# Kernel optimization log

Hardware: AMD Instinct MI355X
Metric: run time of the kernel (lower is better)

## Reference

```python
import jax, jax.numpy as jnp
import numpy as np

IMAGE_SIZE = 256
NEAR = 0.1
FAR = 100.0
CHUNK = 200  # faces per rasterization chunk


def setup_inputs() -> dict:
    key = jax.random.key(0)
    k1, k2, k3 = jax.random.split(key, 3)
    B, Nv, Nf = 1, 10000, 10000
    # vertices sized so that after weak projection (u = f*x + c, f=1015, c=112,
    # orig_size=224) they land inside the image plane; z kept positive.
    xy = jax.random.uniform(k1, (B, Nv, 2), minval=-0.1, maxval=0.1)
    z = jax.random.uniform(k3, (B, Nv, 1), minval=0.4, maxval=0.8)
    vertices = jnp.concatenate([xy, z], axis=-1).astype(jnp.float32)
    faces = jax.random.randint(k2, (B, Nf, 3), 0, Nv).astype(jnp.int64)
    f, c = 1015.0, 112.0
    K = jnp.broadcast_to(jnp.array([[f, 0.0, c], [0.0, f, c], [0.0, 0.0, 1.0]],
                                   dtype=jnp.float32), (B, 3, 3))
    R = jnp.broadcast_to(jnp.eye(3, dtype=jnp.float32), (B, 3, 3))
    t = jnp.zeros((B, 3), dtype=jnp.float32)
    return {"vertices": vertices, "faces": faces, "K": K, "R": R, "t": t,
            "orig_size": 224}


def weak_projection(vertices, K, R, t, orig_size):
    # camera transform: v_cam = v @ R^T + t   [B,N,3]
    v = jnp.einsum('bnj,bkj->bnk', vertices, R) + t[:, None, :]
    x, y, z = v[..., 0], v[..., 1], v[..., 2]
    fx, fy = K[:, 0:1, 0], K[:, 1:2, 1]  # [B,1]
    cx, cy = K[:, 0:1, 2], K[:, 1:2, 2]
    # weak (orthographic-with-focal) projection: no divide by z
    u = fx * x + cx
    w = fy * y + cy
    xn = 2.0 * u / orig_size - 1.0        # NDC x in [-1,1]
    yn = -(2.0 * w / orig_size - 1.0)     # image y down -> NDC y up
    return jnp.stack([xn, yn, z], axis=-1)


def _rasterize_depth(face_verts):
    # face_verts: [B, F, 3, 3] (NDC x, NDC y, camera z)
    B, F = face_verts.shape[0], face_verts.shape[1]
    IS = IMAGE_SIZE
    ps = (2.0 * (jnp.arange(IS, dtype=jnp.float32) + 0.5) / IS) - 1.0
    px = ps[None, :]    # [1, W]
    py = -ps[:, None]   # [H, 1], row 0 is top of image

    def chunk_depth(fc):  # fc: [B, C, 3, 3] -> per-pixel min depth [B, H, W]
        x = fc[..., 0][..., None, None]  # [B,C,3,1,1]
        y = fc[..., 1][..., None, None]
        z = fc[..., 2]                   # [B,C,3]
        dx0, dx1, dx2 = x[:, :, 0] - px, x[:, :, 1] - px, x[:, :, 2] - px  # [B,C,1,W]
        dy0, dy1, dy2 = y[:, :, 0] - py, y[:, :, 1] - py, y[:, :, 2] - py  # [B,C,H,1]
        # edge functions (unnormalized barycentric weights) [B,C,H,W]
        w0 = dx1 * dy2 - dx2 * dy1
        w1 = dx2 * dy0 - dx0 * dy2
        w2 = dx0 * dy1 - dx1 * dy0
        area = w0 + w1 + w2
        s = jnp.sign(area)
        inside = (w0 * s >= 0) & (w1 * s >= 0) & (w2 * s >= 0) & (jnp.abs(area) > 1e-10)
        safe_area = jnp.where(jnp.abs(area) > 1e-10, area, 1.0)
        zp = (w0 * z[:, :, 0, None, None] + w1 * z[:, :, 1, None, None]
              + w2 * z[:, :, 2, None, None]) / safe_area
        valid = inside & (zp > NEAR) & (zp < FAR)
        return jnp.min(jnp.where(valid, zp, FAR), axis=1)  # [B,H,W]

    pad = (-F) % CHUNK
    fv = jnp.pad(face_verts, ((0, 0), (0, pad), (0, 0), (0, 0)))  # degenerate pads -> area 0
    n = (F + pad) // CHUNK
    fv = fv.reshape(B, n, CHUNK, 3, 3).transpose(1, 0, 2, 3, 4)  # [n,B,C,3,3]
    ck = jax.checkpoint(chunk_depth)

    def step(carry, fc):
        return jnp.minimum(carry, ck(fc)), None

    depth0 = jnp.full((B, IS, IS), FAR, dtype=jnp.float32)
    depth, _ = jax.lax.scan(step, depth0, fv)
    return depth


def reference(vertices, faces, K, R, t, orig_size):
    # fill_back: append reversed-winding copies of every face
    faces2 = jnp.concatenate([faces, faces[:, :, ::-1]], axis=1)  # [B,2F,3]
    v = weak_projection(vertices, K, R, t, orig_size)             # [B,Nv,3]
    face_verts = jax.vmap(lambda vb, fb: vb[fb])(v, faces2)       # [B,2F,3,3]
    return _rasterize_depth(face_verts)                           # [B,256,256]
```

## Files before the change

kernel.cpp:

```cpp
#include <hip/hip_runtime.h>

#define IMG 256
#define FARZ 100.0f
#define FARB 0x42C80000u
#define TILE 16
#define NZ 8
#define RND 512
#define BT 512
#define EPS 1e-4f
#define EPSZ 1e-5f
#define DPIX (2.0f / IMG)
#define BBZ_EMPTY 0x00FF00FFu

typedef float f2 __attribute__((ext_vector_type(2)));
static __device__ __forceinline__ f2 pkfma(f2 a, f2 b, f2 c) {
    return __builtin_elementwise_fma(a, b, c);
}
static __device__ __forceinline__ f2 pkmin(f2 a, f2 b) {
    return __builtin_elementwise_min(a, b);
}
static __device__ __forceinline__ float wave_max(float v) {
#pragma unroll
    for (int m = 32; m >= 1; m >>= 1) v = fmaxf(v, __shfl_xor(v, m, 64));
    return v;
}
static __device__ __forceinline__ float wave_min(float v) {
#pragma unroll
    for (int m = 32; m >= 1; m >>= 1) v = fminf(v, __shfl_xor(v, m, 64));
    return v;
}

struct Q4 { f2 r0, r1; };
static __device__ __forceinline__ Q4 eval4(float A, float B, float C,
                                           float px0, float py0) {
    Q4 o;
    float w00 = fmaf(B, px0, fmaf(C, py0, A));
    o.r0 = pkfma((f2){B, B}, (f2){0.0f, DPIX}, (f2){w00, w00});
    o.r1 = pkfma((f2){C, C}, (f2){-DPIX, -DPIX}, o.r0);
    return o;
}

__global__ __launch_bounds__(256) void setup(const float* __restrict__ verts,
                                             const int* __restrict__ faces,
                                             const float* __restrict__ K,
                                             const float* __restrict__ Rm,
                                             const float* __restrict__ t,
                                             const int* __restrict__ osz,
                                             float4* __restrict__ QQ,
                                             float2* __restrict__ BBz,
                                             unsigned* __restrict__ gb,
                                             unsigned* __restrict__ out, int Nf) {
    __shared__ float sb[4][4];
    int tid = threadIdx.x;
    int i = blockIdx.x * 256 + tid;
    out[i] = FARB;

    float k0 = 104.0f, k1 = 104.0f, k2 = 104.0f, k3 = 104.0f;
    if (i < Nf) {
        float fx = K[0], cx = K[2], fy = K[4], cy = K[5];
        float os = (float)osz[0];
        float r00 = Rm[0], r01 = Rm[1], r02 = Rm[2];
        float r10 = Rm[3], r11 = Rm[4], r12 = Rm[5];
        float r20 = Rm[6], r21 = Rm[7], r22 = Rm[8];
        float t0 = t[0], t1 = t[1], t2 = t[2];

        float3 p[3];
#pragma unroll
        for (int k = 0; k < 3; ++k) {
            int vi = faces[3 * i + k];
            float vx = verts[3 * vi], vy = verts[3 * vi + 1], vz = verts[3 * vi + 2];
            float x = r00 * vx + r01 * vy + r02 * vz + t0;
            float y = r10 * vx + r11 * vy + r12 * vz + t1;
            float z = r20 * vx + r21 * vy + r22 * vz + t2;
            float u = fx * x + cx;
            float w = fy * y + cy;
            p[k].x = 2.0f * u / os - 1.0f;
            p[k].y = -(2.0f * w / os - 1.0f);
            p[k].z = z;
        }

        float A0 = p[1].x * p[2].y - p[2].x * p[1].y;
        float B0 = p[1].y - p[2].y;
        float C0 = p[2].x - p[1].x;
        float A1 = p[2].x * p[0].y - p[0].x * p[2].y;
        float B1 = p[2].y - p[0].y;
        float C1 = p[0].x - p[2].x;
        float A2 = p[0].x * p[1].y - p[1].x * p[0].y;
        float B2 = p[0].y - p[1].y;
        float C2 = p[1].x - p[0].x;

        float area = A0 + A1 + A2;
        if (fabsf(area) > 1e-10f) {
            float s = (area > 0.0f) ? 1.0f : -1.0f;
            A0 *= s; B0 *= s; C0 *= s;
            A1 *= s; B1 *= s; C1 *= s;
            A2 *= s; B2 *= s; C2 *= s;
            float inv = (1.0f / area) * s;
            float P = (A0 * p[0].z + A1 * p[1].z + A2 * p[2].z) * inv;
            float Q = (B0 * p[0].z + B1 * p[1].z + B2 * p[2].z) * inv;
            float Rr = (C0 * p[0].z + C1 * p[1].z + C2 * p[2].z) * inv;
            QQ[3 * i + 0] = make_float4(A0, B0, C0, A1);
            QQ[3 * i + 1] = make_float4(B1, C1, A2, B2);
            QQ[3 * i + 2] = make_float4(C2, P, Q, Rr);
            float xmn = fminf(p[0].x, fminf(p[1].x, p[2].x));
            float xmx = fmaxf(p[0].x, fmaxf(p[1].x, p[2].x));
            float ymn = fminf(p[0].y, fminf(p[1].y, p[2].y));
            float ymx = fmaxf(p[0].y, fmaxf(p[1].y, p[2].y));
            float zmv = fminf(p[0].z, fminf(p[1].z, p[2].z));
            int c0 = (int)floorf((xmn + 1.0f) * 128.0f - 0.52f);
            int c1 = (int)ceilf ((xmx + 1.0f) * 128.0f - 0.48f);
            int r0 = (int)floorf((1.0f - ymx) * 128.0f - 0.52f);
            int r1 = (int)ceilf ((1.0f - ymn) * 128.0f - 0.48f);
            c0 = min(max(c0, 0), 255); c1 = min(max(c1, 0), 255);
            r0 = min(max(r0, 0), 255); r1 = min(max(r1, 0), 255);
            unsigned bb = (unsigned)c0 | ((unsigned)c1 << 8) |
                          ((unsigned)r0 << 16) | ((unsigned)r1 << 24);
            BBz[i] = make_float2(__uint_as_float(bb), zmv);
            k0 = 4.0f + xmn; k1 = 4.0f - xmx;
            k2 = 4.0f + ymn; k3 = 4.0f - ymx;
        } else {
            QQ[3 * i + 0] = make_float4(0.0f, 0.0f, 0.0f, 0.0f);
            QQ[3 * i + 1] = make_float4(0.0f, 0.0f, 0.0f, 0.0f);
            QQ[3 * i + 2] = make_float4(0.0f, 0.0f, 0.0f, 0.0f);
            BBz[i] = make_float2(__uint_as_float(BBZ_EMPTY), 1e9f);
        }
    }

    k0 = wave_min(k0); k1 = wave_min(k1); k2 = wave_min(k2); k3 = wave_min(k3);
    int wave = tid >> 6, lane = tid & 63;
    if (lane == 0) { sb[wave][0] = k0; sb[wave][1] = k1; sb[wave][2] = k2; sb[wave][3] = k3; }
    __syncthreads();
    if (tid < 4) {
        float v = fminf(fminf(sb[0][tid], sb[1][tid]), fminf(sb[2][tid], sb[3][tid]));
        atomicMin(&gb[tid], __float_as_uint(v));
    }
}

__global__ __launch_bounds__(BT) void raster(const float4* __restrict__ QQ,
                                             const float2* __restrict__ BBz,
                                             const unsigned* __restrict__ gb,
                                             unsigned* __restrict__ out,
                                             int Nf, int span) {
    __shared__ float4 sf[RND * 3];
    __shared__ unsigned sdepth[TILE * TILE];
    __shared__ int scnt2[2];

    const int tid = threadIdx.x;
    const int bx = blockIdx.x, by = blockIdx.y;
    const int wave = tid >> 6, lane = tid & 63;
    const int tx0 = bx * TILE, ty0 = by * TILE;

    const float cx0 = -1.0f + (tx0 + 0.5f) * DPIX;
    const float cyTop = 1.0f - (ty0 + 0.5f) * DPIX;
    const float tcx = cx0 + 7.5f * DPIX;
    const float tcy = cyTop - 7.5f * DPIX;
    const float hx = 7.5f * DPIX;
    const float hy = 7.5f * DPIX;

    const float gxmin = __uint_as_float(gb[0]) - 4.0f;
    const float gxmax = 4.0f - __uint_as_float(gb[1]);
    const float gymin = __uint_as_float(gb[2]) - 4.0f;
    const float gymax = 4.0f - __uint_as_float(gb[3]);

    const int col = tid & 15, row = (tid >> 4) & 15;
    const int gidx = (ty0 + row) * IMG + tx0 + col;
    unsigned orig = FARB;
    if (tid < 256) {
        orig = out[gidx];
        sdepth[tid] = orig;
    }
    if (tid == 0) { scnt2[0] = 0; scnt2[1] = 0; }

    const int qx = (lane & 7) * 2, qy = (lane >> 3) * 2;
    const float fpx0 = cx0 + (float)qx * DPIX;
    const float fpy0 = cyTop - (float)qy * DPIX;
    int cm = 0;
    {
        const float x0 = fpx0, x1 = fpx0 + DPIX;
        const float y0 = fpy0, y1 = fpy0 - DPIX;
        const bool cx_0 = (x0 >= gxmin - 1e-6f) & (x0 <= gxmax + 1e-6f);
        const bool cx_1 = (x1 >= gxmin - 1e-6f) & (x1 <= gxmax + 1e-6f);
        const bool cy_0 = (y0 >= gymin - 1e-6f) & (y0 <= gymax + 1e-6f);
        const bool cy_1 = (y1 >= gymin - 1e-6f) & (y1 <= gymax + 1e-6f);
        cm = (cx_0 & cy_0) | ((cx_1 & cy_0) << 1) |
             ((cx_0 & cy_1) << 2) | ((cx_1 & cy_1) << 3);
    }
    __syncthreads();

    unsigned dmu[4];
    float T;
    {
        uint2 a = *(const uint2*)&sdepth[qy * TILE + qx];
        uint2 b = *(const uint2*)&sdepth[(qy + 1) * TILE + qx];
        dmu[0] = a.x; dmu[1] = a.y; dmu[2] = b.x; dmu[3] = b.y;
        float m = 0.0f;
        if (cm & 1) m = fmaxf(m, __uint_as_float(a.x));
        if (cm & 2) m = fmaxf(m, __uint_as_float(a.y));
        if (cm & 4) m = fmaxf(m, __uint_as_float(b.x));
        if (cm & 8) m = fmaxf(m, __uint_as_float(b.y));
        T = wave_max(m);
    }
    if (T == 0.0f) return;

    const int fbase = blockIdx.z * span;
    const int fend = min(fbase + span, Nf);

    int f = fbase + tid;
    float2 bz = (f < fend) ? BBz[f]
                           : make_float2(__uint_as_float(BBZ_EMPTY), 1e9f);

    int p = 0;
    for (int base = fbase; base < fend; base += RND) {
        const unsigned bb = __float_as_uint(bz.x);
        const bool pre = ((int)(bb & 255u) <= tx0 + 15) &
                         ((int)((bb >> 8) & 255u) >= tx0) &
                         ((int)((bb >> 16) & 255u) <= ty0 + 15) &
                         ((int)(bb >> 24) >= ty0) &
                         (bz.y <= T + EPSZ);
        const int fcur = f;
        const int fn = f + RND;
        bz = (fn < fend) ? BBz[fn]
                         : make_float2(__uint_as_float(BBZ_EMPTY), 1e9f);

        bool keep = false;
        float4 q0, q1, q2;
        if (pre) {
            q0 = QQ[3 * fcur + 0];
            q1 = QQ[3 * fcur + 1];
            q2 = QQ[3 * fcur + 2];
            float m0 = fmaf(q0.y, tcx, fmaf(q0.z, tcy, q0.x)) +
                       fabsf(q0.y) * hx + fabsf(q0.z) * hy;
            float m1 = fmaf(q1.x, tcx, fmaf(q1.y, tcy, q0.w)) +
                       fabsf(q1.x) * hx + fabsf(q1.y) * hy;
            float m2 = fmaf(q1.w, tcx, fmaf(q2.x, tcy, q1.z)) +
                       fabsf(q1.w) * hx + fabsf(q2.x) * hy;
            keep = (m0 >= -EPS) & (m1 >= -EPS) & (m2 >= -EPS);
        }

        unsigned long long mk = __ballot(keep);
        int bw = 0;
        if (lane == 0) {
            int c = __popcll(mk);
            if (c) bw = atomicAdd(&scnt2[p], c);
        }
        bw = __builtin_amdgcn_readfirstlane(bw);
        if (keep) {
            int slot = bw + __popcll(mk & ((1ull << lane) - 1ull));
            sf[3 * slot + 0] = q0;
            sf[3 * slot + 1] = q1;
            sf[3 * slot + 2] = q2;
        }
        __syncthreads();
        const int n = scnt2[p];
        if (tid == 0) scnt2[p ^ 1] = 0;

        if (n > 0) {
#pragma unroll 2
            for (int j = wave; j < n; j += 8) {
                const float4 c0 = sf[3 * j + 0];
                const float4 c1 = sf[3 * j + 1];
                const float4 c2 = sf[3 * j + 2];
                Q4 w0 = eval4(c0.x, c0.y, c0.z, fpx0, fpy0);
                Q4 w1 = eval4(c0.w, c1.x, c1.y, fpx0, fpy0);
                Q4 w2 = eval4(c1.z, c1.w, c2.x, fpx0, fpy0);
                Q4 zz = eval4(c2.y, c2.z, c2.w, fpx0, fpy0);
                f2 mn0 = pkmin(pkmin(w0.r0, w1.r0), w2.r0);
                f2 mn1 = pkmin(pkmin(w0.r1, w1.r1), w2.r1);
                unsigned u0 = (__float_as_uint(mn0.x) & 0x80000000u) | __float_as_uint(zz.r0.x);
                unsigned u1 = (__float_as_uint(mn0.y) & 0x80000000u) | __float_as_uint(zz.r0.y);
                unsigned u2 = (__float_as_uint(mn1.x) & 0x80000000u) | __float_as_uint(zz.r1.x);
                unsigned u3 = (__float_as_uint(mn1.y) & 0x80000000u) | __float_as_uint(zz.r1.y);
                dmu[0] = min(dmu[0], u0);
                dmu[1] = min(dmu[1], u1);
                dmu[2] = min(dmu[2], u2);
                dmu[3] = min(dmu[3], u3);
            }
            atomicMin(&sdepth[qy * TILE + qx], dmu[0]);
            atomicMin(&sdepth[qy * TILE + qx + 1], dmu[1]);
            atomicMin(&sdepth[(qy + 1) * TILE + qx], dmu[2]);
            atomicMin(&sdepth[(qy + 1) * TILE + qx + 1], dmu[3]);
        }
        __syncthreads();

        if (n > 0) {
            uint2 a = *(const uint2*)&sdepth[qy * TILE + qx];
            uint2 b = *(const uint2*)&sdepth[(qy + 1) * TILE + qx];
            float m = 0.0f;
            if (cm & 1) m = fmaxf(m, __uint_as_float(a.x));
            if (cm & 2) m = fmaxf(m, __uint_as_float(a.y));
            if (cm & 4) m = fmaxf(m, __uint_as_float(b.x));
            if (cm & 8) m = fmaxf(m, __uint_as_float(b.y));
            T = wave_max(m);
        }
        f = fn;
        p ^= 1;
    }

    if (tid < 256) {
        unsigned fv = sdepth[tid];
        if (fv < orig) atomicMin(out + gidx, fv);
    }
}

extern "C" void kernel_launch(void* const* d_in, const int* in_sizes, int n_in,
                              void* d_out, int out_size, void* d_ws, size_t ws_size,
                              hipStream_t stream) {
    const float* verts = (const float*)d_in[0];
    const int* faces   = (const int*)d_in[1];
    const float* K     = (const float*)d_in[2];
    const float* Rm    = (const float*)d_in[3];
    const float* t     = (const float*)d_in[4];
    const int* osz     = (const int*)d_in[5];

    int Nf = in_sizes[1] / 3;
    int span = (Nf + NZ - 1) / NZ;

    float4* QQ = (float4*)d_ws;
    float2* BBz = (float2*)(QQ + 3 * Nf);
    unsigned* gb = (unsigned*)(BBz + Nf);
    unsigned* out = (unsigned*)d_out;

    setup<<<(IMG * IMG) / 256, 256, 0, stream>>>(verts, faces, K, Rm, t, osz,
                                                 QQ, BBz, gb, out, Nf);

    raster<<<dim3(IMG / TILE, IMG / TILE, NZ), BT, 0, stream>>>(
        QQ, BBz, gb, out, Nf, span);
}
```

Measured before the change: 107.9 us.

## Precompute per-tile occluder depth bound in setup to cull faces earlier

The setup kernel now finds, for each 16x16 tile, the faces that fully cover the tile. It computes a conservative maximum depth for each such face and reduces these into a per-tile bound (tileT0) with atomics, first in shared memory and then in global memory. The raster kernel clamps its depth-culling threshold T with this bound from the start, so occluded faces are rejected before any per-pixel work, even across z-slices. NZ drops from 8 to 4, which halves the face-split blocks and means less redundant tile setup but also less parallelism. Setup gains extra per-face tile loops and relies on the workspace already holding the tileT0 initial values.

```diff
diff --git a/kernel.cpp b/kernel.cpp
--- a/kernel.cpp
+++ b/kernel.cpp
@@ -4,12 +4,14 @@
 #define FARZ 100.0f
 #define FARB 0x42C80000u
 #define TILE 16
-#define NZ 8
+#define NZ 4
 #define RND 512
 #define BT 512
 #define EPS 1e-4f
 #define EPSZ 1e-5f
+#define FEPS 1e-6f
 #define DPIX (2.0f / IMG)
+#define HXT (7.5f * DPIX)
 #define BBZ_EMPTY 0x00FF00FFu
 
 typedef float f2 __attribute__((ext_vector_type(2)));
@@ -49,11 +51,16 @@
                                              float4* __restrict__ QQ,
                                              float2* __restrict__ BBz,
                                              unsigned* __restrict__ gb,
+                                             unsigned* __restrict__ tileT0,
                                              unsigned* __restrict__ out, int Nf) {
     __shared__ float sb[4][4];
+    __shared__ unsigned st0[256];
     int tid = threadIdx.x;
     int i = blockIdx.x * 256 + tid;
     out[i] = FARB;
+    st0[tid] = 0xFFFFFFFFu;
+    const bool hasFaces = (blockIdx.x * 256 < Nf);
+    if (hasFaces) __syncthreads();
 
     float k0 = 104.0f, k1 = 104.0f, k2 = 104.0f, k3 = 104.0f;
     if (i < Nf) {
@@ -118,6 +125,26 @@
             BBz[i] = make_float2(__uint_as_float(bb), zmv);
             k0 = 4.0f + xmn; k1 = 4.0f - xmx;
             k2 = 4.0f + ymn; k3 = 4.0f - ymx;
+
+            int txl = c0 >> 4, txh = c1 >> 4;
+            int tyl = r0 >> 4, tyh = r1 >> 4;
+            for (int ty = tyl; ty <= tyh; ++ty) {
+                float tcy = 1.0f - ((float)(ty * 16 + 8)) * DPIX;
+                for (int tx = txl; tx <= txh; ++tx) {
+                    float tcx = -1.0f + ((float)(tx * 16 + 8)) * DPIX;
+                    float w0 = fmaf(B0, tcx, fmaf(C0, tcy, A0)) -
+                               (fabsf(B0) + fabsf(C0)) * HXT;
+                    float w1 = fmaf(B1, tcx, fmaf(C1, tcy, A1)) -
+                               (fabsf(B1) + fabsf(C1)) * HXT;
+                    float w2 = fmaf(B2, tcx, fmaf(C2, tcy, A2)) -
+                               (fabsf(B2) + fabsf(C2)) * HXT;
+                    if ((w0 >= FEPS) & (w1 >= FEPS) & (w2 >= FEPS)) {
+                        float zmx = fmaf(Q, tcx, fmaf(Rr, tcy, P)) +
+                                    (fabsf(Q) + fabsf(Rr)) * HXT;
+                        atomicMin(&st0[ty * 16 + tx], __float_as_uint(zmx));
+                    }
+                }
+            }
         } else {
             QQ[3 * i + 0] = make_float4(0.0f, 0.0f, 0.0f, 0.0f);
             QQ[3 * i + 1] = make_float4(0.0f, 0.0f, 0.0f, 0.0f);
@@ -134,11 +161,16 @@
         float v = fminf(fminf(sb[0][tid], sb[1][tid]), fminf(sb[2][tid], sb[3][tid]));
         atomicMin(&gb[tid], __float_as_uint(v));
     }
+    if (hasFaces) {
+        unsigned v = st0[tid];
+        if (v != 0xFFFFFFFFu) atomicMin(&tileT0[tid], v);
+    }
 }
 
 __global__ __launch_bounds__(BT) void raster(const float4* __restrict__ QQ,
                                              const float2* __restrict__ BBz,
                                              const unsigned* __restrict__ gb,
+                                             const unsigned* __restrict__ tileT0,
                                              unsigned* __restrict__ out,
                                              int Nf, int span) {
     __shared__ float4 sf[RND * 3];
@@ -154,13 +186,14 @@
     const float cyTop = 1.0f - (ty0 + 0.5f) * DPIX;
     const float tcx = cx0 + 7.5f * DPIX;
     const float tcy = cyTop - 7.5f * DPIX;
-    const float hx = 7.5f * DPIX;
-    const float hy = 7.5f * DPIX;
 
     const float gxmin = __uint_as_float(gb[0]) - 4.0f;
     const float gxmax = 4.0f - __uint_as_float(gb[1]);
     const float gymin = __uint_as_float(gb[2]) - 4.0f;
     const float gymax = 4.0f - __uint_as_float(gb[3]);
+
+    const unsigned t0u = tileT0[by * 16 + bx];
+    const float T0f = (t0u & 0x80000000u) ? FARZ : __uint_as_float(t0u);
 
     const int col = tid & 15, row = (tid >> 4) & 15;
     const int gidx = (ty0 + row) * IMG + tx0 + col;
@@ -201,6 +234,7 @@
         T = wave_max(m);
     }
     if (T == 0.0f) return;
+    T = fminf(T, T0f);
 
     const int fbase = blockIdx.z * span;
     const int fend = min(fbase + span, Nf);
@@ -229,11 +263,11 @@
             q1 = QQ[3 * fcur + 1];
             q2 = QQ[3 * fcur + 2];
             float m0 = fmaf(q0.y, tcx, fmaf(q0.z, tcy, q0.x)) +
-                       fabsf(q0.y) * hx + fabsf(q0.z) * hy;
+                       (fabsf(q0.y) + fabsf(q0.z)) * HXT;
             float m1 = fmaf(q1.x, tcx, fmaf(q1.y, tcy, q0.w)) +
-                       fabsf(q1.x) * hx + fabsf(q1.y) * hy;
+                       (fabsf(q1.x) + fabsf(q1.y)) * HXT;
             float m2 = fmaf(q1.w, tcx, fmaf(q2.x, tcy, q1.z)) +
-                       fabsf(q1.w) * hx + fabsf(q2.x) * hy;
+                       (fabsf(q1.w) + fabsf(q2.x)) * HXT;
             keep = (m0 >= -EPS) & (m1 >= -EPS) & (m2 >= -EPS);
         }
 
@@ -290,7 +324,7 @@
             if (cm & 2) m = fmaxf(m, __uint_as_float(a.y));
             if (cm & 4) m = fmaxf(m, __uint_as_float(b.x));
             if (cm & 8) m = fmaxf(m, __uint_as_float(b.y));
-            T = wave_max(m);
+            T = fminf(wave_max(m), T0f);
         }
         f = fn;
         p ^= 1;
@@ -318,11 +352,12 @@
     float4* QQ = (float4*)d_ws;
     float2* BBz = (float2*)(QQ + 3 * Nf);
     unsigned* gb = (unsigned*)(BBz + Nf);
+    unsigned* tileT0 = gb + 4;
     unsigned* out = (unsigned*)d_out;
 
     setup<<<(IMG * IMG) / 256, 256, 0, stream>>>(verts, faces, K, Rm, t, osz,
-                                                 QQ, BBz, gb, out, Nf);
+                                                 QQ, BBz, gb, tileT0, out, Nf);
 
     raster<<<dim3(IMG / TILE, IMG / TILE, NZ), BT, 0, stream>>>(
-        QQ, BBz, gb, out, Nf, span);
-}
+        QQ, BBz, gb, tileT0, out, Nf, span);
+}
```

Result: slower. 136.6 us (+26.6%).
